# Optimization experiments

Measured on AMD Instinct MI355X. Metric: run time of the kernel, lower is better.

The kernel has to match this reference:

```python
import jax, jax.numpy as jnp
import numpy as np

H, HKV, DH = 16, 8, 128
G = H // HKV
EPS = 1e-6
ROPE_THETA = 1000000.0


def _rms_norm(x, w):
    # RMSNorm over last dim (head_dim)
    var = jnp.mean(x * x, axis=-1, keepdims=True)
    return x * jax.lax.rsqrt(var + EPS) * w


def _rotate_half(x):
    x1, x2 = jnp.split(x, 2, axis=-1)
    return jnp.concatenate([-x2, x1], axis=-1)


def setup_inputs() -> dict:
    key = jax.random.key(0)
    ks = jax.random.split(key, 5)
    B, T, D = 2, 2048, 2048
    s = 0.02
    return {
        "x": jax.random.normal(ks[0], (B, T, D), jnp.float32),
        "wq": jax.random.normal(ks[1], (H * DH, D), jnp.float32) * s,
        "wk": jax.random.normal(ks[2], (HKV * DH, D), jnp.float32) * s,
        "wv": jax.random.normal(ks[3], (HKV * DH, D), jnp.float32) * s,
        "wo": jax.random.normal(ks[4], (D, H * DH), jnp.float32) * s,
        "q_norm_w": jnp.ones((DH,), jnp.float32),
        "k_norm_w": jnp.ones((DH,), jnp.float32),
    }


def reference(x, wq, wk, wv, wo, q_norm_w, k_norm_w):
    B, T, D = x.shape
    # projections (nn.Linear: y = x @ W^T)
    q = (x @ wq.T).reshape(B, T, H, DH).transpose(0, 2, 1, 3)      # [B,H,T,Dh]
    k = (x @ wk.T).reshape(B, T, HKV, DH).transpose(0, 2, 1, 3)    # [B,Hkv,T,Dh]
    v = (x @ wv.T).reshape(B, T, HKV, DH).transpose(0, 2, 1, 3)    # [B,Hkv,T,Dh]

    # QK RMSNorm
    q = _rms_norm(q, q_norm_w)
    k = _rms_norm(k, k_norm_w)

    # RoPE (half-split style), positions 0..T-1
    inv_freq = 1.0 / (ROPE_THETA ** (jnp.arange(0, DH, 2, dtype=jnp.float32) / DH))
    freqs = jnp.arange(T, dtype=jnp.float32)[:, None] * inv_freq[None, :]   # [T,Dh/2]
    emb = jnp.concatenate([freqs, freqs], axis=-1)                           # [T,Dh]
    cos = jnp.cos(emb)[None, None, :, :]
    sin = jnp.sin(emb)[None, None, :, :]
    q = q * cos + _rotate_half(q) * sin
    k = k * cos + _rotate_half(k) * sin

    # GQA attention with fp32 scores and causal mask
    qg = q.reshape(B, HKV, G, T, DH)
    scores = jnp.einsum("bhgtd,bhkd->bhgtk", qg.astype(jnp.float32),
                        k.astype(jnp.float32)) / jnp.sqrt(jnp.float32(DH))
    causal = jnp.tril(jnp.ones((T, T), dtype=bool))[None, None, None, :, :]
    scores = jnp.where(causal, scores, jnp.finfo(jnp.float32).min)
    attn = jax.nn.softmax(scores, axis=-1).astype(x.dtype)
    ctx = jnp.einsum("bhgtk,bhkd->bhgtd", attn, v)                            # [B,Hkv,G,T,Dh]
    out = ctx.reshape(B, H, T, DH).transpose(0, 2, 1, 3).reshape(B, T, H * DH)
    return out @ wo.T
```

## Files before the change

### kernel.cpp

```cpp
#include <hip/hip_runtime.h>
#include <cstdint>

#define Hq 16
#define HKVn 8
#define DHn 128
#define Tn 2048
#define Bn 2
#define Dm 2048
#define BT (Bn*Tn)

typedef __attribute__((ext_vector_type(8))) short bfrag8;
typedef __attribute__((ext_vector_type(4))) float facc4;
typedef __attribute__((ext_vector_type(4))) _Float16 f16x4;
typedef __attribute__((ext_vector_type(8))) _Float16 f16x8;
typedef __attribute__((ext_vector_type(8))) unsigned short us8;

__device__ __forceinline__ unsigned short f2bf(float f) {
    union { float f; unsigned int u; } v; v.f = f;
    unsigned int u = v.u;
    unsigned int r = (u + 0x7FFFu + ((u >> 16) & 1u)) >> 16;
    return (unsigned short)r;
}
__device__ __forceinline__ float bf2f(unsigned short u) {
    union { unsigned int u; float f; } v; v.u = ((unsigned int)u) << 16;
    return v.f;
}

__global__ __launch_bounds__(256) void cvt_all(const float* __restrict__ x,
                                               const float* __restrict__ wq,
                                               const float* __restrict__ wk,
                                               const float* __restrict__ wv,
                                               const float* __restrict__ wo,
                                               unsigned short* __restrict__ x_bf,
                                               unsigned short* __restrict__ wqkv_bf,
                                               unsigned short* __restrict__ wo_bf) {
    int i = blockIdx.x * 256 + threadIdx.x;
    const float4* src; ushort4* dst;
    if (i < 2097152)      { src = (const float4*)x  + i;            dst = (ushort4*)x_bf + i; }
    else if (i < 3145728) { src = (const float4*)wq + (i-2097152);  dst = (ushort4*)wqkv_bf + (i-2097152); }
    else if (i < 3670016) { src = (const float4*)wk + (i-3145728);  dst = (ushort4*)wqkv_bf + 1048576 + (i-3145728); }
    else if (i < 4194304) { src = (const float4*)wv + (i-3670016);  dst = (ushort4*)wqkv_bf + 1572864 + (i-3670016); }
    else                  { src = (const float4*)wo + (i-4194304);  dst = (ushort4*)wo_bf + (i-4194304); }
    float4 v = *src;
    ushort4 y;
    y.x = f2bf(v.x); y.y = f2bf(v.y); y.z = f2bf(v.z); y.w = f2bf(v.w);
    *dst = y;
}

__device__ __forceinline__ size_t koff_tiled(int t, int d) {
    int kc = (t >> 4) & 3, l15 = t & 15;
    int f = d >> 5, qd = (d >> 3) & 3, j = d & 7;
    return (size_t)(t >> 6) * 8192 + ((((kc * 4 + f) * 64 + qd * 16 + l15) << 3) + j);
}

__global__ __launch_bounds__(256) void gemm_bt(const unsigned short* __restrict__ A,
                                               const unsigned short* __restrict__ Bm,
                                               float* __restrict__ C,
                                               int M, int N, int K) {
    __shared__ char smem[32768];
    int tid = threadIdx.x;
    int w = tid >> 6, lane = tid & 63, quad = lane >> 4, l15 = lane & 15;
    int wr = w >> 1, wc = w & 1;
    int rowBase = blockIdx.y * 128, colBase = blockIdx.x * 128;
    facc4 acc[4][4];
#pragma unroll
    for (int i = 0; i < 4; i++)
#pragma unroll
        for (int j = 0; j < 4; j++) acc[i][j] = facc4{0.f, 0.f, 0.f, 0.f};

    for (int k0 = 0; k0 < K; k0 += 64) {
        __syncthreads();
#pragma unroll
        for (int i4 = 0; i4 < 4; i4++) {
            int c = i4 * 256 + tid;
            int r = c >> 3, kkg = (c & 7) ^ (r & 7);
            const unsigned short* ga = A + (size_t)(rowBase + r) * K + k0 + kkg * 8;
            __builtin_amdgcn_global_load_lds((const __attribute__((address_space(1))) void*)ga,
                (__attribute__((address_space(3))) void*)(smem + i4 * 4096 + w * 1024), 16, 0, 0);
            const unsigned short* gb = Bm + (size_t)(colBase + r) * K + k0 + kkg * 8;
            __builtin_amdgcn_global_load_lds((const __attribute__((address_space(1))) void*)gb,
                (__attribute__((address_space(3))) void*)(smem + 16384 + i4 * 4096 + w * 1024), 16, 0, 0);
        }
        __syncthreads();
#pragma unroll
        for (int kh = 0; kh < 2; kh++) {
            bfrag8 af[4], bf[4];
#pragma unroll
            for (int i = 0; i < 4; i++) {
                int row = wr * 64 + i * 16 + l15;
                int ch = row * 8 + ((kh * 4 + quad) ^ (row & 7));
                af[i] = *(const bfrag8*)(smem + ch * 16);
            }
#pragma unroll
            for (int j = 0; j < 4; j++) {
                int row = wc * 64 + j * 16 + l15;
                int ch = row * 8 + ((kh * 4 + quad) ^ (row & 7));
                bf[j] = *(const bfrag8*)(smem + 16384 + ch * 16);
            }
#pragma unroll
            for (int i = 0; i < 4; i++)
#pragma unroll
                for (int j = 0; j < 4; j++)
                    acc[i][j] = __builtin_amdgcn_mfma_f32_16x16x32_bf16(af[i], bf[j], acc[i][j], 0, 0, 0);
        }
    }
#pragma unroll
    for (int i = 0; i < 4; i++)
#pragma unroll
        for (int j = 0; j < 4; j++)
#pragma unroll
            for (int r = 0; r < 4; r++) {
                int row = rowBase + wr * 64 + i * 16 + quad * 4 + r;
                int col = colBase + wc * 64 + j * 16 + l15;
                C[(size_t)row * N + col] = acc[i][j][r];
            }
}

__global__ __launch_bounds__(256) void gemm_qkv_fused(const unsigned short* __restrict__ A,
                                                      const unsigned short* __restrict__ Bm,
                                                      const float* __restrict__ qw,
                                                      const float* __restrict__ kw,
                                                      unsigned short* __restrict__ q_bf,
                                                      unsigned short* __restrict__ k_bf,
                                                      _Float16* __restrict__ vT) {
    __shared__ char smem[35840];
    const int K = 2048, Nn = 4096;
    int tid = threadIdx.x;
    int w = tid >> 6, lane = tid & 63, quad = lane >> 4, l15 = lane & 15;
    int wr = w >> 1, wc = w & 1;
    int bx = blockIdx.x;
    int rowBase = blockIdx.y * 128, colBase = bx * 128;
    (void)Nn;
    facc4 acc[4][4];
#pragma unroll
    for (int i = 0; i < 4; i++)
#pragma unroll
        for (int j = 0; j < 4; j++) acc[i][j] = facc4{0.f, 0.f, 0.f, 0.f};

    for (int k0 = 0; k0 < K; k0 += 64) {
        __syncthreads();
#pragma unroll
        for (int i4 = 0; i4 < 4; i4++) {
            int c = i4 * 256 + tid;
            int r = c >> 3, kkg = (c & 7) ^ (r & 7);
            const unsigned short* ga = A + (size_t)(rowBase + r) * K + k0 + kkg * 8;
            __builtin_amdgcn_global_load_lds((const __attribute__((address_space(1))) void*)ga,
                (__attribute__((address_space(3))) void*)(smem + i4 * 4096 + w * 1024), 16, 0, 0);
            const unsigned short* gb = Bm + (size_t)(colBase + r) * K + k0 + kkg * 8;
            __builtin_amdgcn_global_load_lds((const __attribute__((address_space(1))) void*)gb,
                (__attribute__((address_space(3))) void*)(smem + 16384 + i4 * 4096 + w * 1024), 16, 0, 0);
        }
        __syncthreads();
#pragma unroll
        for (int kh = 0; kh < 2; kh++) {
            bfrag8 af[4], bf[4];
#pragma unroll
            for (int i = 0; i < 4; i++) {
                int row = wr * 64 + i * 16 + l15;
                int ch = row * 8 + ((kh * 4 + quad) ^ (row & 7));
                af[i] = *(const bfrag8*)(smem + ch * 16);
            }
#pragma unroll
            for (int j = 0; j < 4; j++) {
                int row = wc * 64 + j * 16 + l15;
                int ch = row * 8 + ((kh * 4 + quad) ^ (row & 7));
                bf[j] = *(const bfrag8*)(smem + 16384 + ch * 16);
            }
#pragma unroll
            for (int i = 0; i < 4; i++)
#pragma unroll
                for (int j = 0; j < 4; j++)
                    acc[i][j] = __builtin_amdgcn_mfma_f32_16x16x32_bf16(af[i], bf[j], acc[i][j], 0, 0, 0);
        }
    }

    if (bx >= 24) {
        int hv = bx - 24;
        int gt0 = rowBase + wr * 64;
        int bb = gt0 >> 11;
        int t64 = (gt0 & 2047) >> 6;
        _Float16* base = vT + ((size_t)(bb * 8 + hv) * 32 + t64) * 8192;
#pragma unroll
        for (int i = 0; i < 4; i++) {
            int kcp = i >> 1, hh = i & 1;
#pragma unroll
            for (int j = 0; j < 4; j++) {
                int dblk = wc * 4 + j;
                f16x4 pv;
#pragma unroll
                for (int r = 0; r < 4; r++) pv[r] = (_Float16)acc[i][j][r];
                *(f16x4*)(base + (((dblk * 2 + kcp) * 64 + quad * 16 + l15) * 8) + hh * 4) = pv;
            }
        }
        return;
    }

    const float* wn = (bx < 16) ? qw : kw;
    const float osc = (bx < 16) ? (0.08838834764831845f * 1.4426950408889634f) : 1.0f;
    float* sums = (float*)(smem + 34816);
    float ssum[4][4];
#pragma unroll
    for (int i = 0; i < 4; i++)
#pragma unroll
        for (int r = 0; r < 4; r++) {
            float s = 0.f;
#pragma unroll
            for (int j = 0; j < 4; j++) s += acc[i][j][r] * acc[i][j][r];
            s += __shfl_xor(s, 1); s += __shfl_xor(s, 2);
            s += __shfl_xor(s, 4); s += __shfl_xor(s, 8);
            ssum[i][r] = s;
        }
    if (l15 == 0) {
#pragma unroll
        for (int i = 0; i < 4; i++)
#pragma unroll
            for (int r = 0; r < 4; r++)
                sums[wc * 128 + wr * 64 + i * 16 + quad * 4 + r] = ssum[i][r];
    }
    __syncthreads();
    unsigned short* tile = (unsigned short*)smem;
    float wcol[4];
#pragma unroll
    for (int j = 0; j < 4; j++) wcol[j] = wn[wc * 64 + j * 16 + l15];
#pragma unroll
    for (int i = 0; i < 4; i++)
#pragma unroll
        for (int r = 0; r < 4; r++) {
            int row = wr * 64 + i * 16 + quad * 4 + r;
            float tot = sums[row] + sums[128 + row];
            float inv = rsqrtf(tot * (1.0f / 128.0f) + 1e-6f);
#pragma unroll
            for (int j = 0; j < 4; j++)
                tile[row * 136 + wc * 64 + j * 16 + l15] = f2bf(acc[i][j][r] * inv * wcol[j]);
        }
    __syncthreads();
    {
        int row = tid >> 1, d0 = (tid & 1) * 32;
        int gt = rowBase + row;
        int t = gt & 2047, bb = gt >> 11;
        unsigned short* qrow = q_bf + ((size_t)(bb * 16 + bx) * 2048 + t) * 128;
        unsigned short* kplane = k_bf + (size_t)(bb * 8 + (bx - 16)) * 2048 * 128;
        float tf = (float)t;
#pragma unroll
        for (int dc = 0; dc < 32; dc += 8) {
            int db = d0 + dc;
            us8 n0u = *(const us8*)(tile + row * 136 + db);
            us8 n1u = *(const us8*)(tile + row * 136 + db + 64);
            us8 p0, p1;
#pragma unroll
            for (int e = 0; e < 8; e++) {
                float fr = exp2f(-(float)(db + e) * 0.3114307588956902f);
                float sv, cv;
                __sincosf(tf * fr, &sv, &cv);
                float a0 = bf2f(n0u[e]), a1 = bf2f(n1u[e]);
                p0[e] = f2bf((a0 * cv - a1 * sv) * osc);
                p1[e] = f2bf((a1 * cv + a0 * sv) * osc);
            }
            if (bx < 16) {
                *(us8*)(qrow + db) = p0;
                *(us8*)(qrow + db + 64) = p1;
            } else {
                *(us8*)(kplane + koff_tiled(t, db)) = p0;
                *(us8*)(kplane + koff_tiled(t, db + 64)) = p1;
            }
        }
    }
}

__global__ __launch_bounds__(256, 2) void attn_kernel(const unsigned short* __restrict__ q_bf,
                                                      const unsigned short* __restrict__ k_glob,
                                                      const _Float16* __restrict__ v_glob,
                                                      unsigned short* __restrict__ ctx) {
    __shared__ char smem[65536];
    int tid = threadIdx.x;
    int w = tid >> 6, lane = tid & 63, quad = lane >> 4, l15 = lane & 15;
    int bid = blockIdx.x;
    int u = bid & 255, halfg = bid >> 8;
    int j = u & 7, h = (u >> 3) & 15, b = (u >> 7) & 1;
    int qblk = halfg ? j : 15 - j;
    int hkv = h >> 1;
    int qb = qblk * 128;
    int qw0 = qb + w * 32;

    const unsigned short* qp = q_bf + (size_t)(b * Hq + h) * Tn * 128;
    const unsigned short* ktile = k_glob + (size_t)(b * HKVn + hkv) * 32 * 8192;
    const _Float16* vtile = v_glob + (size_t)(b * HKVn + hkv) * 32 * 8192;

    bfrag8 qf[2][4];
#pragma unroll
    for (int g = 0; g < 2; g++) {
        int row = qw0 + g * 16 + l15;
#pragma unroll
        for (int f = 0; f < 4; f++)
            qf[g][f] = *(const bfrag8*)(qp + (size_t)row * 128 + f * 32 + quad * 8);
    }

    facc4 o0[8], o1[8];
#pragma unroll
    for (int jj = 0; jj < 8; jj++) { o0[jj] = facc4{0.f,0.f,0.f,0.f}; o1[jj] = facc4{0.f,0.f,0.f,0.f}; }
    float m0 = -__builtin_inff(), m1 = -__builtin_inff(), l0 = 0.f, l1 = 0.f;

    int nkb = qb / 64 + 2;
#pragma unroll
    for (int i = 0; i < 4; i++) {
        const unsigned short* gk = ktile + (size_t)(i * 256 + tid) * 8;
        __builtin_amdgcn_global_load_lds((const __attribute__((address_space(1))) void*)gk,
            (__attribute__((address_space(3))) void*)(smem + i * 4096 + w * 1024), 16, 0, 0);
        const _Float16* gv = vtile + (size_t)(i * 256 + tid) * 8;
        __builtin_amdgcn_global_load_lds((const __attribute__((address_space(1))) void*)gv,
            (__attribute__((address_space(3))) void*)(smem + 16384 + i * 4096 + w * 1024), 16, 0, 0);
    }

    for (int ib = 0; ib < nkb; ib++) {
        int kb = ib * 64;
        __syncthreads();
        if (ib + 1 < nkb) {
            char* nb = smem + ((ib + 1) & 1) * 32768;
#pragma unroll
            for (int i = 0; i < 4; i++) {
                const unsigned short* gk = ktile + (size_t)(ib + 1) * 8192 + (i * 256 + tid) * 8;
                __builtin_amdgcn_global_load_lds((const __attribute__((address_space(1))) void*)gk,
                    (__attribute__((address_space(3))) void*)(nb + i * 4096 + w * 1024), 16, 0, 0);
                const _Float16* gv = vtile + (size_t)(ib + 1) * 8192 + (i * 256 + tid) * 8;
                __builtin_amdgcn_global_load_lds((const __attribute__((address_space(1))) void*)gv,
                    (__attribute__((address_space(3))) void*)(nb + 16384 + i * 4096 + w * 1024), 16, 0, 0);
            }
        }
        char* cb = smem + (ib & 1) * 32768;
        if (kb <= qw0 + 31) {
            facc4 s0[4], s1[4];
#pragma unroll
            for (int kc = 0; kc < 4; kc++) {
                bfrag8 kf[4];
#pragma unroll
                for (int f = 0; f < 4; f++)
                    kf[f] = *(const bfrag8*)(cb + (((kc * 4 + f) * 64 + lane) << 4));
                facc4 a = facc4{0.f,0.f,0.f,0.f}, bq = facc4{0.f,0.f,0.f,0.f};
#pragma unroll
                for (int f = 0; f < 4; f++) {
                    a  = __builtin_amdgcn_mfma_f32_16x16x32_bf16(kf[f], qf[0][f], a, 0, 0, 0);
                    bq = __builtin_amdgcn_mfma_f32_16x16x32_bf16(kf[f], qf[1][f], bq, 0, 0, 0);
                }
                s0[kc] = a; s1[kc] = bq;
            }
            if (kb + 63 > qw0) {
                int q0 = qw0 + l15, q1 = q0 + 16;
#pragma unroll
                for (int kc = 0; kc < 4; kc++)
#pragma unroll
                    for (int r = 0; r < 4; r++) {
                        int k = kb + kc * 16 + quad * 4 + r;
                        if (k > q0) s0[kc][r] = -__builtin_inff();
                        if (k > q1) s1[kc][r] = -__builtin_inff();
                    }
            }
            float mx0 = s0[0][0], mx1 = s1[0][0];
#pragma unroll
            for (int kc = 0; kc < 4; kc++)
#pragma unroll
                for (int r = 0; r < 4; r++) {
                    mx0 = fmaxf(mx0, s0[kc][r]); mx1 = fmaxf(mx1, s1[kc][r]);
                }
            mx0 = fmaxf(mx0, __shfl_xor(mx0, 16)); mx0 = fmaxf(mx0, __shfl_xor(mx0, 32));
            mx1 = fmaxf(mx1, __shfl_xor(mx1, 16)); mx1 = fmaxf(mx1, __shfl_xor(mx1, 32));
            float mn0 = fmaxf(m0, mx0), mn1 = fmaxf(m1, mx1);
            float alpha0 = exp2f(m0 - mn0), alpha1 = exp2f(m1 - mn1);
            m0 = mn0; m1 = mn1;
            float rs0 = 0.f, rs1 = 0.f;
#pragma unroll
            for (int kc = 0; kc < 4; kc++)
#pragma unroll
                for (int r = 0; r < 4; r++) {
                    s0[kc][r] = exp2f(s0[kc][r] - m0); rs0 += s0[kc][r];
                    s1[kc][r] = exp2f(s1[kc][r] - m1); rs1 += s1[kc][r];
                }
            rs0 += __shfl_xor(rs0, 16); rs0 += __shfl_xor(rs0, 32);
            rs1 += __shfl_xor(rs1, 16); rs1 += __shfl_xor(rs1, 32);
            l0 = l0 * alpha0 + rs0; l1 = l1 * alpha1 + rs1;
#pragma unroll
            for (int jj = 0; jj < 8; jj++)
#pragma unroll
                for (int r = 0; r < 4; r++) { o0[jj][r] *= alpha0; o1[jj][r] *= alpha1; }
            f16x4 pb0[4], pb1[4];
#pragma unroll
            for (int kc = 0; kc < 4; kc++) {
                pb0[kc] = f16x4{(_Float16)s0[kc][0], (_Float16)s0[kc][1],
                                (_Float16)s0[kc][2], (_Float16)s0[kc][3]};
                pb1[kc] = f16x4{(_Float16)s1[kc][0], (_Float16)s1[kc][1],
                                (_Float16)s1[kc][2], (_Float16)s1[kc][3]};
            }
#pragma unroll
            for (int kcp = 0; kcp < 2; kcp++)
#pragma unroll
                for (int dblk = 0; dblk < 8; dblk++) {
                    f16x8 vv = *(const f16x8*)(cb + 16384 + (((dblk * 2 + kcp) * 64 + lane) << 4));
                    f16x4 a0 = f16x4{vv[0], vv[1], vv[2], vv[3]};
                    f16x4 a1 = f16x4{vv[4], vv[5], vv[6], vv[7]};
                    o0[dblk] = __builtin_amdgcn_mfma_f32_16x16x16f16(a0, pb0[kcp*2],   o0[dblk], 0, 0, 0);
                    o0[dblk] = __builtin_amdgcn_mfma_f32_16x16x16f16(a1, pb0[kcp*2+1], o0[dblk], 0, 0, 0);
                    o1[dblk] = __builtin_amdgcn_mfma_f32_16x16x16f16(a0, pb1[kcp*2],   o1[dblk], 0, 0, 0);
                    o1[dblk] = __builtin_amdgcn_mfma_f32_16x16x16f16(a1, pb1[kcp*2+1], o1[dblk], 0, 0, 0);
                }
        }
    }
    float inv0 = 1.0f / l0, inv1 = 1.0f / l1;
#pragma unroll
    for (int g = 0; g < 2; g++) {
        int q = qw0 + g * 16 + l15;
        float invl = g ? inv1 : inv0;
#pragma unroll
        for (int dblk = 0; dblk < 8; dblk++) {
            facc4 ov = g ? o1[dblk] : o0[dblk];
            ushort4 st;
            st.x = f2bf(ov[0] * invl); st.y = f2bf(ov[1] * invl);
            st.z = f2bf(ov[2] * invl); st.w = f2bf(ov[3] * invl);
            *(ushort4*)(ctx + ((size_t)(b * Tn + q)) * 2048 + h * 128 + dblk * 16 + quad * 4) = st;
        }
    }
}

extern "C" void kernel_launch(void* const* d_in, const int* in_sizes, int n_in,
                              void* d_out, int out_size, void* d_ws, size_t ws_size,
                              hipStream_t stream) {
    (void)in_sizes; (void)n_in; (void)out_size; (void)ws_size;
    const float* x  = (const float*)d_in[0];
    const float* wq = (const float*)d_in[1];
    const float* wk = (const float*)d_in[2];
    const float* wv = (const float*)d_in[3];
    const float* wo = (const float*)d_in[4];
    const float* qw = (const float*)d_in[5];
    const float* kw = (const float*)d_in[6];
    float* out = (float*)d_out;
    char* ws = (char*)d_ws;

    unsigned short* x_bf    = (unsigned short*)(ws);
    unsigned short* wqkv_bf = (unsigned short*)(ws + 16777216);
    unsigned short* wo_bf   = (unsigned short*)(ws + 33554432);
    unsigned short* q_bf    = (unsigned short*)(ws + 41943040);
    unsigned short* k_bf    = (unsigned short*)(ws + 58720256);
    _Float16*       vT_f16  = (_Float16*)(ws + 67108864);
    unsigned short* ctx_bf  = (unsigned short*)(ws + 75497472);

    cvt_all<<<20480, 256, 0, stream>>>(x, wq, wk, wv, wo, x_bf, wqkv_bf, wo_bf);
    gemm_qkv_fused<<<dim3(32, 32), 256, 0, stream>>>(x_bf, wqkv_bf, qw, kw, q_bf, k_bf, vT_f16);
    attn_kernel<<<512, 256, 0, stream>>>(q_bf, k_bf, vT_f16, ctx_bf);
    gemm_bt<<<dim3(16, 32), 256, 0, stream>>>(ctx_bf, wo_bf, out, 4096, 2048, 2048);
}
```

Before: 331.7 us.

## Use RoPE sin/cos lookup table and read K/V tiles directly from global in attention

The RoPE epilogue in the QKV GEMM now reads cos/sin from a lookup table built inside the conversion kernel, replacing per-element exp2f and sincos. The attention kernel drops its double-buffered LDS staging of K/V tiles and barriers, and each wave loads its K/V fragments straight from global memory (relying on cache). Each wave also computes its own causal trip count, so waves skip key blocks beyond their own query rows. The risks are redundant global/L2 traffic, since the four waves in a block now each fetch the same K/V tiles, and exposed load latency with no prefetch.

```diff
diff --git a/kernel.cpp b/kernel.cpp
--- a/kernel.cpp
+++ b/kernel.cpp
@@ -33,8 +33,20 @@
                                                const float* __restrict__ wo,
                                                unsigned short* __restrict__ x_bf,
                                                unsigned short* __restrict__ wqkv_bf,
-                                               unsigned short* __restrict__ wo_bf) {
+                                               unsigned short* __restrict__ wo_bf,
+                                               float* __restrict__ lut) {
     int i = blockIdx.x * 256 + threadIdx.x;
+    if (i >= 5242880) {
+        int ii = i - 5242880;
+        int t = ii >> 6, d = ii & 63;
+        float fr = exp2f(-(float)d * 0.3114307588956902f);
+        float ang = (float)t * fr;
+        float sv, cv;
+        __sincosf(ang, &sv, &cv);
+        lut[t * 128 + d] = cv;
+        lut[t * 128 + 64 + d] = sv;
+        return;
+    }
     const float4* src; ushort4* dst;
     if (i < 2097152)      { src = (const float4*)x  + i;            dst = (ushort4*)x_bf + i; }
     else if (i < 3145728) { src = (const float4*)wq + (i-2097152);  dst = (ushort4*)wqkv_bf + (i-2097152); }
@@ -120,17 +132,17 @@
                                                       const unsigned short* __restrict__ Bm,
                                                       const float* __restrict__ qw,
                                                       const float* __restrict__ kw,
+                                                      const float* __restrict__ lut,
                                                       unsigned short* __restrict__ q_bf,
                                                       unsigned short* __restrict__ k_bf,
                                                       _Float16* __restrict__ vT) {
     __shared__ char smem[35840];
-    const int K = 2048, Nn = 4096;
+    const int K = 2048;
     int tid = threadIdx.x;
     int w = tid >> 6, lane = tid & 63, quad = lane >> 4, l15 = lane & 15;
     int wr = w >> 1, wc = w & 1;
     int bx = blockIdx.x;
     int rowBase = blockIdx.y * 128, colBase = bx * 128;
-    (void)Nn;
     facc4 acc[4][4];
 #pragma unroll
     for (int i = 0; i < 4; i++)
@@ -240,21 +252,22 @@
         int t = gt & 2047, bb = gt >> 11;
         unsigned short* qrow = q_bf + ((size_t)(bb * 16 + bx) * 2048 + t) * 128;
         unsigned short* kplane = k_bf + (size_t)(bb * 8 + (bx - 16)) * 2048 * 128;
-        float tf = (float)t;
+        const float* lc = lut + t * 128;
 #pragma unroll
         for (int dc = 0; dc < 32; dc += 8) {
             int db = d0 + dc;
             us8 n0u = *(const us8*)(tile + row * 136 + db);
             us8 n1u = *(const us8*)(tile + row * 136 + db + 64);
+            float4 cA = *(const float4*)(lc + db), cB = *(const float4*)(lc + db + 4);
+            float4 sA = *(const float4*)(lc + 64 + db), sB = *(const float4*)(lc + 64 + db + 4);
+            float cv[8] = {cA.x, cA.y, cA.z, cA.w, cB.x, cB.y, cB.z, cB.w};
+            float sv[8] = {sA.x, sA.y, sA.z, sA.w, sB.x, sB.y, sB.z, sB.w};
             us8 p0, p1;
 #pragma unroll
             for (int e = 0; e < 8; e++) {
-                float fr = exp2f(-(float)(db + e) * 0.3114307588956902f);
-                float sv, cv;
-                __sincosf(tf * fr, &sv, &cv);
                 float a0 = bf2f(n0u[e]), a1 = bf2f(n1u[e]);
-                p0[e] = f2bf((a0 * cv - a1 * sv) * osc);
-                p1[e] = f2bf((a1 * cv + a0 * sv) * osc);
+                p0[e] = f2bf((a0 * cv[e] - a1 * sv[e]) * osc);
+                p1[e] = f2bf((a1 * cv[e] + a0 * sv[e]) * osc);
             }
             if (bx < 16) {
                 *(us8*)(qrow + db) = p0;
@@ -271,7 +284,6 @@
                                                       const unsigned short* __restrict__ k_glob,
                                                       const _Float16* __restrict__ v_glob,
                                                       unsigned short* __restrict__ ctx) {
-    __shared__ char smem[65536];
     int tid = threadIdx.x;
     int w = tid >> 6, lane = tid & 63, quad = lane >> 4, l15 = lane & 15;
     int bid = blockIdx.x;
@@ -300,108 +312,84 @@
     for (int jj = 0; jj < 8; jj++) { o0[jj] = facc4{0.f,0.f,0.f,0.f}; o1[jj] = facc4{0.f,0.f,0.f,0.f}; }
     float m0 = -__builtin_inff(), m1 = -__builtin_inff(), l0 = 0.f, l1 = 0.f;
 
-    int nkb = qb / 64 + 2;
-#pragma unroll
-    for (int i = 0; i < 4; i++) {
-        const unsigned short* gk = ktile + (size_t)(i * 256 + tid) * 8;
-        __builtin_amdgcn_global_load_lds((const __attribute__((address_space(1))) void*)gk,
-            (__attribute__((address_space(3))) void*)(smem + i * 4096 + w * 1024), 16, 0, 0);
-        const _Float16* gv = vtile + (size_t)(i * 256 + tid) * 8;
-        __builtin_amdgcn_global_load_lds((const __attribute__((address_space(1))) void*)gv,
-            (__attribute__((address_space(3))) void*)(smem + 16384 + i * 4096 + w * 1024), 16, 0, 0);
-    }
-
+    int nkb = (qw0 >> 6) + 1;
     for (int ib = 0; ib < nkb; ib++) {
         int kb = ib * 64;
-        __syncthreads();
-        if (ib + 1 < nkb) {
-            char* nb = smem + ((ib + 1) & 1) * 32768;
-#pragma unroll
-            for (int i = 0; i < 4; i++) {
-                const unsigned short* gk = ktile + (size_t)(ib + 1) * 8192 + (i * 256 + tid) * 8;
-                __builtin_amdgcn_global_load_lds((const __attribute__((address_space(1))) void*)gk,
-                    (__attribute__((address_space(3))) void*)(nb + i * 4096 + w * 1024), 16, 0, 0);
-                const _Float16* gv = vtile + (size_t)(ib + 1) * 8192 + (i * 256 + tid) * 8;
-                __builtin_amdgcn_global_load_lds((const __attribute__((address_space(1))) void*)gv,
-                    (__attribute__((address_space(3))) void*)(nb + 16384 + i * 4096 + w * 1024), 16, 0, 0);
-            }
-        }
-        char* cb = smem + (ib & 1) * 32768;
-        if (kb <= qw0 + 31) {
-            facc4 s0[4], s1[4];
-#pragma unroll
-            for (int kc = 0; kc < 4; kc++) {
-                bfrag8 kf[4];
-#pragma unroll
-                for (int f = 0; f < 4; f++)
-                    kf[f] = *(const bfrag8*)(cb + (((kc * 4 + f) * 64 + lane) << 4));
-                facc4 a = facc4{0.f,0.f,0.f,0.f}, bq = facc4{0.f,0.f,0.f,0.f};
-#pragma unroll
-                for (int f = 0; f < 4; f++) {
-                    a  = __builtin_amdgcn_mfma_f32_16x16x32_bf16(kf[f], qf[0][f], a, 0, 0, 0);
-                    bq = __builtin_amdgcn_mfma_f32_16x16x32_bf16(kf[f], qf[1][f], bq, 0, 0, 0);
+        const unsigned short* kt = ktile + (size_t)ib * 8192;
+        const _Float16* vt = vtile + (size_t)ib * 8192;
+        facc4 s0[4], s1[4];
+#pragma unroll
+        for (int kc = 0; kc < 4; kc++) {
+            bfrag8 kf[4];
+#pragma unroll
+            for (int f = 0; f < 4; f++)
+                kf[f] = *(const bfrag8*)(kt + ((kc * 4 + f) * 64 + lane) * 8);
+            facc4 a = facc4{0.f,0.f,0.f,0.f}, bq = facc4{0.f,0.f,0.f,0.f};
+#pragma unroll
+            for (int f = 0; f < 4; f++) {
+                a  = __builtin_amdgcn_mfma_f32_16x16x32_bf16(kf[f], qf[0][f], a, 0, 0, 0);
+                bq = __builtin_amdgcn_mfma_f32_16x16x32_bf16(kf[f], qf[1][f], bq, 0, 0, 0);
+            }
+            s0[kc] = a; s1[kc] = bq;
+        }
+        if (kb + 63 > qw0) {
+            int q0 = qw0 + l15, q1 = q0 + 16;
+#pragma unroll
+            for (int kc = 0; kc < 4; kc++)
+#pragma unroll
+                for (int r = 0; r < 4; r++) {
+                    int k = kb + kc * 16 + quad * 4 + r;
+                    if (k > q0) s0[kc][r] = -__builtin_inff();
+                    if (k > q1) s1[kc][r] = -__builtin_inff();
                 }
-                s0[kc] = a; s1[kc] = bq;
-            }
-            if (kb + 63 > qw0) {
-                int q0 = qw0 + l15, q1 = q0 + 16;
-#pragma unroll
-                for (int kc = 0; kc < 4; kc++)
-#pragma unroll
-                    for (int r = 0; r < 4; r++) {
-                        int k = kb + kc * 16 + quad * 4 + r;
-                        if (k > q0) s0[kc][r] = -__builtin_inff();
-                        if (k > q1) s1[kc][r] = -__builtin_inff();
-                    }
-            }
-            float mx0 = s0[0][0], mx1 = s1[0][0];
-#pragma unroll
-            for (int kc = 0; kc < 4; kc++)
-#pragma unroll
-                for (int r = 0; r < 4; r++) {
-                    mx0 = fmaxf(mx0, s0[kc][r]); mx1 = fmaxf(mx1, s1[kc][r]);
-                }
-            mx0 = fmaxf(mx0, __shfl_xor(mx0, 16)); mx0 = fmaxf(mx0, __shfl_xor(mx0, 32));
-            mx1 = fmaxf(mx1, __shfl_xor(mx1, 16)); mx1 = fmaxf(mx1, __shfl_xor(mx1, 32));
-            float mn0 = fmaxf(m0, mx0), mn1 = fmaxf(m1, mx1);
-            float alpha0 = exp2f(m0 - mn0), alpha1 = exp2f(m1 - mn1);
-            m0 = mn0; m1 = mn1;
-            float rs0 = 0.f, rs1 = 0.f;
-#pragma unroll
-            for (int kc = 0; kc < 4; kc++)
-#pragma unroll
-                for (int r = 0; r < 4; r++) {
-                    s0[kc][r] = exp2f(s0[kc][r] - m0); rs0 += s0[kc][r];
-                    s1[kc][r] = exp2f(s1[kc][r] - m1); rs1 += s1[kc][r];
-                }
-            rs0 += __shfl_xor(rs0, 16); rs0 += __shfl_xor(rs0, 32);
-            rs1 += __shfl_xor(rs1, 16); rs1 += __shfl_xor(rs1, 32);
-            l0 = l0 * alpha0 + rs0; l1 = l1 * alpha1 + rs1;
-#pragma unroll
-            for (int jj = 0; jj < 8; jj++)
-#pragma unroll
-                for (int r = 0; r < 4; r++) { o0[jj][r] *= alpha0; o1[jj][r] *= alpha1; }
-            f16x4 pb0[4], pb1[4];
-#pragma unroll
-            for (int kc = 0; kc < 4; kc++) {
-                pb0[kc] = f16x4{(_Float16)s0[kc][0], (_Float16)s0[kc][1],
-                                (_Float16)s0[kc][2], (_Float16)s0[kc][3]};
-                pb1[kc] = f16x4{(_Float16)s1[kc][0], (_Float16)s1[kc][1],
-                                (_Float16)s1[kc][2], (_Float16)s1[kc][3]};
-            }
-#pragma unroll
-            for (int kcp = 0; kcp < 2; kcp++)
-#pragma unroll
-                for (int dblk = 0; dblk < 8; dblk++) {
-                    f16x8 vv = *(const f16x8*)(cb + 16384 + (((dblk * 2 + kcp) * 64 + lane) << 4));
-                    f16x4 a0 = f16x4{vv[0], vv[1], vv[2], vv[3]};
-                    f16x4 a1 = f16x4{vv[4], vv[5], vv[6], vv[7]};
-                    o0[dblk] = __builtin_amdgcn_mfma_f32_16x16x16f16(a0, pb0[kcp*2],   o0[dblk], 0, 0, 0);
-                    o0[dblk] = __builtin_amdgcn_mfma_f32_16x16x16f16(a1, pb0[kcp*2+1], o0[dblk], 0, 0, 0);
-                    o1[dblk] = __builtin_amdgcn_mfma_f32_16x16x16f16(a0, pb1[kcp*2],   o1[dblk], 0, 0, 0);
-                    o1[dblk] = __builtin_amdgcn_mfma_f32_16x16x16f16(a1, pb1[kcp*2+1], o1[dblk], 0, 0, 0);
-                }
-        }
+        }
+        float mx0 = s0[0][0], mx1 = s1[0][0];
+#pragma unroll
+        for (int kc = 0; kc < 4; kc++)
+#pragma unroll
+            for (int r = 0; r < 4; r++) {
+                mx0 = fmaxf(mx0, s0[kc][r]); mx1 = fmaxf(mx1, s1[kc][r]);
+            }
+        mx0 = fmaxf(mx0, __shfl_xor(mx0, 16)); mx0 = fmaxf(mx0, __shfl_xor(mx0, 32));
+        mx1 = fmaxf(mx1, __shfl_xor(mx1, 16)); mx1 = fmaxf(mx1, __shfl_xor(mx1, 32));
+        float mn0 = fmaxf(m0, mx0), mn1 = fmaxf(m1, mx1);
+        float alpha0 = exp2f(m0 - mn0), alpha1 = exp2f(m1 - mn1);
+        m0 = mn0; m1 = mn1;
+        float rs0 = 0.f, rs1 = 0.f;
+#pragma unroll
+        for (int kc = 0; kc < 4; kc++)
+#pragma unroll
+            for (int r = 0; r < 4; r++) {
+                s0[kc][r] = exp2f(s0[kc][r] - m0); rs0 += s0[kc][r];
+                s1[kc][r] = exp2f(s1[kc][r] - m1); rs1 += s1[kc][r];
+            }
+        rs0 += __shfl_xor(rs0, 16); rs0 += __shfl_xor(rs0, 32);
+        rs1 += __shfl_xor(rs1, 16); rs1 += __shfl_xor(rs1, 32);
+        l0 = l0 * alpha0 + rs0; l1 = l1 * alpha1 + rs1;
+#pragma unroll
+        for (int jj = 0; jj < 8; jj++)
+#pragma unroll
+            for (int r = 0; r < 4; r++) { o0[jj][r] *= alpha0; o1[jj][r] *= alpha1; }
+        f16x4 pb0[4], pb1[4];
+#pragma unroll
+        for (int kc = 0; kc < 4; kc++) {
+            pb0[kc] = f16x4{(_Float16)s0[kc][0], (_Float16)s0[kc][1],
+                            (_Float16)s0[kc][2], (_Float16)s0[kc][3]};
+            pb1[kc] = f16x4{(_Float16)s1[kc][0], (_Float16)s1[kc][1],
+                            (_Float16)s1[kc][2], (_Float16)s1[kc][3]};
+        }
+#pragma unroll
+        for (int kcp = 0; kcp < 2; kcp++)
+#pragma unroll
+            for (int dblk = 0; dblk < 8; dblk++) {
+                f16x8 vv = *(const f16x8*)(vt + ((dblk * 2 + kcp) * 64 + lane) * 8);
+                f16x4 a0 = f16x4{vv[0], vv[1], vv[2], vv[3]};
+                f16x4 a1 = f16x4{vv[4], vv[5], vv[6], vv[7]};
+                o0[dblk] = __builtin_amdgcn_mfma_f32_16x16x16f16(a0, pb0[kcp*2],   o0[dblk], 0, 0, 0);
+                o0[dblk] = __builtin_amdgcn_mfma_f32_16x16x16f16(a1, pb0[kcp*2+1], o0[dblk], 0, 0, 0);
+                o1[dblk] = __builtin_amdgcn_mfma_f32_16x16x16f16(a0, pb1[kcp*2],   o1[dblk], 0, 0, 0);
+                o1[dblk] = __builtin_amdgcn_mfma_f32_16x16x16f16(a1, pb1[kcp*2+1], o1[dblk], 0, 0, 0);
+            }
     }
     float inv0 = 1.0f / l0, inv1 = 1.0f / l1;
 #pragma unroll
@@ -440,9 +428,10 @@
     unsigned short* k_bf    = (unsigned short*)(ws + 58720256);
     _Float16*       vT_f16  = (_Float16*)(ws + 67108864);
     unsigned short* ctx_bf  = (unsigned short*)(ws + 75497472);
-
-    cvt_all<<<20480, 256, 0, stream>>>(x, wq, wk, wv, wo, x_bf, wqkv_bf, wo_bf);
-    gemm_qkv_fused<<<dim3(32, 32), 256, 0, stream>>>(x_bf, wqkv_bf, qw, kw, q_bf, k_bf, vT_f16);
+    float*          lut     = (float*)(ws + 92274688);
+
+    cvt_all<<<20992, 256, 0, stream>>>(x, wq, wk, wv, wo, x_bf, wqkv_bf, wo_bf, lut);
+    gemm_qkv_fused<<<dim3(32, 32), 256, 0, stream>>>(x_bf, wqkv_bf, qw, kw, lut, q_bf, k_bf, vT_f16);
     attn_kernel<<<512, 256, 0, stream>>>(q_bf, k_bf, vT_f16, ctx_bf);
     gemm_bt<<<dim3(16, 32), 256, 0, stream>>>(ctx_bf, wo_bf, out, 4096, 2048, 2048);
 }
```

After: 507.1 us. +52.9%, slower.
